# Kernel tuning notes

Measured on AMD Instinct MI355X. Metric: run time of the kernel, lower is better.

Reference implementation:

```python
import jax, jax.numpy as jnp
import numpy as np

N_POINTS = 2048
N_EVENTS = 2_000_000
N_QUAD = 10           # midpoint Riemann samples for the non-event integral
NON_EVENT_WEIGHT = 1.0
EPS = 1e-12           # numerical floor inside sqrt (mirrors torch PairwiseDistance eps)


def setup_inputs() -> dict:
    key = jax.random.key(0)
    k1, k2, k3, k4 = jax.random.split(key, 4)
    # learned parameters, init uniform(-0.25, 0.25) as in init_vector
    z0 = jax.random.uniform(k1, (N_POINTS, 2), minval=-0.25, maxval=0.25)
    v0 = jax.random.uniform(k2, (N_POINTS, 2), minval=-0.25, maxval=0.25)
    beta = jnp.asarray(0.0, jnp.float32)  # background intensity parameter
    # event data: columns [u, v, t] split into int pairs and float times
    data_uv = jax.random.randint(k3, (N_EVENTS, 2), 0, N_POINTS).astype(jnp.int32)
    data_t = jax.random.uniform(k4, (N_EVENTS,), dtype=jnp.float32)
    # all node pairs, lower triangle offset=-1 (matches torch.tril_indices)
    iu, ju = np.tril_indices(N_POINTS, k=-1)
    pair_u = jnp.asarray(iu, jnp.int32)
    pair_v = jnp.asarray(ju, jnp.int32)
    t0 = jnp.asarray(0.0, jnp.float32)
    tn = jnp.asarray(1.0, jnp.float32)
    return dict(z0=z0, v0=v0, beta=beta, data_t=data_t, t0=t0, tn=tn,
                data_uv=data_uv, pair_u=pair_u, pair_v=pair_v)


def reference(z0, v0, beta, data_t, t0, tn, data_uv, pair_u, pair_v):
    # --- event term: sum over events of log lambda_uv(t) = beta - ||z_u(t)-z_v(t)|| ---
    u, v = data_uv[:, 0], data_uv[:, 1]
    # z_i(t) = z0_i + v0_i * t  (constant velocity); difference vector per event [E,2]
    dz = (z0[u] - z0[v]) + (v0[u] - v0[v]) * data_t[:, None]
    event_dist = jnp.sqrt(jnp.sum(dz * dz, axis=-1) + EPS)
    event_intensity = jnp.sum(beta - event_dist)

    # --- non-event term: integral over [t0,tn] of lambda_uv(t) for every node pair ---
    # midpoint Riemann rule with N_QUAD samples
    ts = t0 + (jnp.arange(N_QUAD, dtype=jnp.float32) + 0.5) * (tn - t0) / N_QUAD
    dt = (tn - t0) / N_QUAD
    dz0 = z0[pair_u] - z0[pair_v]          # [P,2]
    dv0 = v0[pair_u] - v0[pair_v]          # [P,2]
    dp = dz0[None] + dv0[None] * ts[:, None, None]   # [T,P,2]
    pair_dist = jnp.sqrt(jnp.sum(dp * dp, axis=-1) + EPS)  # [T,P]
    non_event_intensity = dt * jnp.sum(jnp.exp(beta - pair_dist))

    return event_intensity - NON_EVENT_WEIGHT * non_event_intensity
```

## Files before the change

### kernel.cpp

```cpp
#include <hip/hip_runtime.h>

#define BLOCK   256
#define EB      512
#define TILE    64
#define NQUAD   10
#define EPSF    1e-12f

__global__ __launch_bounds__(BLOCK) void cvm_fused_kernel(
    const float* __restrict__ z0, const float* __restrict__ v0,
    const float* __restrict__ beta_p, const float* __restrict__ data_t,
    const float* __restrict__ t0_p, const float* __restrict__ tn_p,
    const int* __restrict__ data_uv,
    float* __restrict__ partials,
    int n_points, int n_events)
{
    __shared__ float4 smem[2048];
    __shared__ float sred[4];

    const int tid = threadIdx.x;
    const int b   = blockIdx.x;
    float acc = 0.0f;

    if (b < EB) {
        const float2* z2 = (const float2*)z0;
        const float2* v2 = (const float2*)v0;
        for (int k = tid; k < n_points; k += BLOCK) {
            float2 z = z2[k];
            float2 v = v2[k];
            smem[k] = make_float4(z.x, z.y, v.x, v.y);
        }
        __syncthreads();

        const int2* uv = (const int2*)data_uv;
        for (int e = b * BLOCK + tid; e < n_events; e += EB * BLOCK) {
            int2  p  = uv[e];
            float t  = data_t[e];
            float4 Pu = smem[p.x];
            float4 Pv = smem[p.y];
            float dx = (Pu.x - Pv.x) + (Pu.z - Pv.z) * t;
            float dy = (Pu.y - Pv.y) + (Pu.w - Pv.w) * t;
            acc += sqrtf(dx * dx + dy * dy + EPSF);
        }
    } else {
        int p  = b - EB;
        int ti = (int)((sqrtf(8.0f * (float)p + 1.0f) - 1.0f) * 0.5f);
        while ((ti + 1) * (ti + 2) / 2 <= p) ti++;
        while (ti * (ti + 1) / 2 > p)        ti--;
        int tj = p - ti * (ti + 1) / 2;
        int I0 = ti * TILE, J0 = tj * TILE;

        float* sI = (float*)smem;
        float* sJ = sI + 4 * TILE;
        if (tid < 2 * TILE) {
            int   side = tid >> 6;
            int   l    = tid & 63;
            int   g    = (side ? J0 : I0) + l;
            float* s   = side ? sJ : sI;
            s[0 * TILE + l] = z0[2 * g];
            s[1 * TILE + l] = z0[2 * g + 1];
            s[2 * TILE + l] = v0[2 * g];
            s[3 * TILE + l] = v0[2 * g + 1];
        }
        __syncthreads();

        float beta = *beta_p, t0 = *t0_p, tn = *tn_p;
        float dt = (tn - t0) * (1.0f / NQUAD);

        int il = tid & 63;
        int w  = tid >> 6;
        int gi = I0 + il;

        float zix = sI[0 * TILE + il], ziy = sI[1 * TILE + il];
        float vix = sI[2 * TILE + il], viy = sI[3 * TILE + il];

        bool diag = (ti == tj);
        for (int k = 0; k < 16; ++k) {
            int jl = w + 4 * k;
            int gj = J0 + jl;
            float dzx = zix - sJ[0 * TILE + jl];
            float dzy = ziy - sJ[1 * TILE + jl];
            float dvx = vix - sJ[2 * TILE + jl];
            float dvy = viy - sJ[3 * TILE + jl];
            if (!diag || gi > gj) {
                float s = 0.0f;
                #pragma unroll
                for (int q = 0; q < NQUAD; ++q) {
                    float tq = t0 + ((float)q + 0.5f) * dt;
                    float dx = dzx + dvx * tq;
                    float dy = dzy + dvy * tq;
                    float d  = sqrtf(dx * dx + dy * dy + EPSF);
                    s += __expf(beta - d);
                }
                acc += s;
            }
        }
    }

    #pragma unroll
    for (int off = 32; off > 0; off >>= 1)
        acc += __shfl_down(acc, off, 64);
    int wave = tid >> 6, lane = tid & 63;
    if (lane == 0) sred[wave] = acc;
    __syncthreads();
    if (tid == 0)
        partials[b] = sred[0] + sred[1] + sred[2] + sred[3];
}

__global__ __launch_bounds__(BLOCK) void cvm_finalize_kernel(
    const float* __restrict__ partials, int total_blocks,
    const float* __restrict__ beta_p, const float* __restrict__ t0_p,
    const float* __restrict__ tn_p,
    float* __restrict__ out, int n_events)
{
    __shared__ float s_e[4], s_p[4];
    float se = 0.0f, sp = 0.0f;
    for (int i = threadIdx.x; i < total_blocks; i += BLOCK) {
        float v = partials[i];
        if (i < EB) se += v; else sp += v;
    }
    #pragma unroll
    for (int off = 32; off > 0; off >>= 1) {
        se += __shfl_down(se, off, 64);
        sp += __shfl_down(sp, off, 64);
    }
    int wave = threadIdx.x >> 6, lane = threadIdx.x & 63;
    if (lane == 0) { s_e[wave] = se; s_p[wave] = sp; }
    __syncthreads();
    if (threadIdx.x == 0) {
        se = s_e[0] + s_e[1] + s_e[2] + s_e[3];
        sp = s_p[0] + s_p[1] + s_p[2] + s_p[3];
        float beta = *beta_p, t0 = *t0_p, tn = *tn_p;
        float dt = (tn - t0) * (1.0f / NQUAD);
        out[0] = ((float)n_events * beta - se) - dt * sp;
    }
}

extern "C" void kernel_launch(void* const* d_in, const int* in_sizes, int n_in,
                              void* d_out, int out_size, void* d_ws, size_t ws_size,
                              hipStream_t stream)
{
    const float* z0      = (const float*)d_in[0];
    const float* v0      = (const float*)d_in[1];
    const float* beta_p  = (const float*)d_in[2];
    const float* data_t  = (const float*)d_in[3];
    const float* t0_p    = (const float*)d_in[4];
    const float* tn_p    = (const float*)d_in[5];
    const int*   data_uv = (const int*)d_in[6];

    int n_points = in_sizes[0] / 2;
    int n_events = in_sizes[3];
    int nt       = n_points / TILE;
    int pt       = nt * (nt + 1) / 2;
    int total    = EB + pt;

    float* partials = (float*)d_ws;
    float* out      = (float*)d_out;

    cvm_fused_kernel<<<total, BLOCK, 0, stream>>>(
        z0, v0, beta_p, data_t, t0_p, tn_p, data_uv,
        partials, n_points, n_events);
    cvm_finalize_kernel<<<1, BLOCK, 0, stream>>>(
        partials, total, beta_p, t0_p, tn_p, out, n_events);
}
```

Measured before the change: 116.1 us.

## Give every block a slice of both event and pair work, atomic final reduce

Replaces the split of 512 event blocks plus 528 pair-tile blocks with 1040 uniform blocks. Each block loads the full point table, handles a strided slice of events, and, if its index is below the pair-tile count, one pair tile. The finalize kernel is removed in favour of a memset and per-block atomicAdd, and exp(beta) is factored out of the quadrature loop. It also switches to the raw hardware sqrt builtin. The aim is better load balance and one fewer launch, at the cost of every block loading the 32KB table and nondeterministic float atomic summation.

```diff
diff --git a/kernel.cpp b/kernel.cpp
--- a/kernel.cpp
+++ b/kernel.cpp
@@ -1,86 +1,73 @@
 #include <hip/hip_runtime.h>
 
 #define BLOCK   256
-#define EB      512
 #define TILE    64
 #define NQUAD   10
 #define EPSF    1e-12f
+#define NTOTAL  1040
 
-__global__ __launch_bounds__(BLOCK) void cvm_fused_kernel(
+__global__ __launch_bounds__(BLOCK) void cvm_kernel(
     const float* __restrict__ z0, const float* __restrict__ v0,
     const float* __restrict__ beta_p, const float* __restrict__ data_t,
     const float* __restrict__ t0_p, const float* __restrict__ tn_p,
     const int* __restrict__ data_uv,
-    float* __restrict__ partials,
-    int n_points, int n_events)
+    float* __restrict__ out,
+    int n_points, int n_events, int pair_tiles)
 {
-    __shared__ float4 smem[2048];
-    __shared__ float sred[4];
+    __shared__ float4 table[2048];
+    __shared__ float sred[8];
 
     const int tid = threadIdx.x;
     const int b   = blockIdx.x;
-    float acc = 0.0f;
 
-    if (b < EB) {
-        const float2* z2 = (const float2*)z0;
-        const float2* v2 = (const float2*)v0;
-        for (int k = tid; k < n_points; k += BLOCK) {
-            float2 z = z2[k];
-            float2 v = v2[k];
-            smem[k] = make_float4(z.x, z.y, v.x, v.y);
-        }
-        __syncthreads();
+    const float2* z2 = (const float2*)z0;
+    const float2* v2 = (const float2*)v0;
+    for (int k = tid; k < n_points; k += BLOCK) {
+        float2 z = z2[k];
+        float2 v = v2[k];
+        table[k] = make_float4(z.x, z.y, v.x, v.y);
+    }
+    __syncthreads();
 
-        const int2* uv = (const int2*)data_uv;
-        for (int e = b * BLOCK + tid; e < n_events; e += EB * BLOCK) {
-            int2  p  = uv[e];
-            float t  = data_t[e];
-            float4 Pu = smem[p.x];
-            float4 Pv = smem[p.y];
-            float dx = (Pu.x - Pv.x) + (Pu.z - Pv.z) * t;
-            float dy = (Pu.y - Pv.y) + (Pu.w - Pv.w) * t;
-            acc += sqrtf(dx * dx + dy * dy + EPSF);
-        }
-    } else {
-        int p  = b - EB;
-        int ti = (int)((sqrtf(8.0f * (float)p + 1.0f) - 1.0f) * 0.5f);
+    const float beta = *beta_p, t0 = *t0_p, tn = *tn_p;
+    const float dt   = (tn - t0) * (1.0f / NQUAD);
+
+    float acc_e = 0.0f;
+    const int2* uv = (const int2*)data_uv;
+    for (int e = b * BLOCK + tid; e < n_events; e += NTOTAL * BLOCK) {
+        int2  p  = uv[e];
+        float t  = data_t[e];
+        float4 Pu = table[p.x];
+        float4 Pv = table[p.y];
+        float dx = (Pu.x - Pv.x) + (Pu.z - Pv.z) * t;
+        float dy = (Pu.y - Pv.y) + (Pu.w - Pv.w) * t;
+        acc_e += __builtin_amdgcn_sqrtf(dx * dx + dy * dy + EPSF);
+    }
+
+    float acc_p = 0.0f;
+    if (b < pair_tiles) {
+        int p  = b;
+        int ti = (int)((__builtin_amdgcn_sqrtf(8.0f * (float)p + 1.0f) - 1.0f) * 0.5f);
         while ((ti + 1) * (ti + 2) / 2 <= p) ti++;
         while (ti * (ti + 1) / 2 > p)        ti--;
         int tj = p - ti * (ti + 1) / 2;
         int I0 = ti * TILE, J0 = tj * TILE;
 
-        float* sI = (float*)smem;
-        float* sJ = sI + 4 * TILE;
-        if (tid < 2 * TILE) {
-            int   side = tid >> 6;
-            int   l    = tid & 63;
-            int   g    = (side ? J0 : I0) + l;
-            float* s   = side ? sJ : sI;
-            s[0 * TILE + l] = z0[2 * g];
-            s[1 * TILE + l] = z0[2 * g + 1];
-            s[2 * TILE + l] = v0[2 * g];
-            s[3 * TILE + l] = v0[2 * g + 1];
-        }
-        __syncthreads();
-
-        float beta = *beta_p, t0 = *t0_p, tn = *tn_p;
-        float dt = (tn - t0) * (1.0f / NQUAD);
-
         int il = tid & 63;
         int w  = tid >> 6;
         int gi = I0 + il;
 
-        float zix = sI[0 * TILE + il], ziy = sI[1 * TILE + il];
-        float vix = sI[2 * TILE + il], viy = sI[3 * TILE + il];
+        float4 Pi = table[I0 + il];
+        bool diag = (ti == tj);
 
-        bool diag = (ti == tj);
         for (int k = 0; k < 16; ++k) {
             int jl = w + 4 * k;
             int gj = J0 + jl;
-            float dzx = zix - sJ[0 * TILE + jl];
-            float dzy = ziy - sJ[1 * TILE + jl];
-            float dvx = vix - sJ[2 * TILE + jl];
-            float dvy = viy - sJ[3 * TILE + jl];
+            float4 Pj = table[J0 + jl];
+            float dzx = Pi.x - Pj.x;
+            float dzy = Pi.y - Pj.y;
+            float dvx = Pi.z - Pj.z;
+            float dvy = Pi.w - Pj.w;
             if (!diag || gi > gj) {
                 float s = 0.0f;
                 #pragma unroll
@@ -88,50 +75,28 @@
                     float tq = t0 + ((float)q + 0.5f) * dt;
                     float dx = dzx + dvx * tq;
                     float dy = dzy + dvy * tq;
-                    float d  = sqrtf(dx * dx + dy * dy + EPSF);
-                    s += __expf(beta - d);
+                    float d  = __builtin_amdgcn_sqrtf(dx * dx + dy * dy + EPSF);
+                    s += __expf(-d);
                 }
-                acc += s;
+                acc_p += s;
             }
         }
     }
 
     #pragma unroll
-    for (int off = 32; off > 0; off >>= 1)
-        acc += __shfl_down(acc, off, 64);
+    for (int off = 32; off > 0; off >>= 1) {
+        acc_e += __shfl_down(acc_e, off, 64);
+        acc_p += __shfl_down(acc_p, off, 64);
+    }
     int wave = tid >> 6, lane = tid & 63;
-    if (lane == 0) sred[wave] = acc;
+    if (lane == 0) { sred[wave] = acc_e; sred[4 + wave] = acc_p; }
     __syncthreads();
-    if (tid == 0)
-        partials[b] = sred[0] + sred[1] + sred[2] + sred[3];
-}
-
-__global__ __launch_bounds__(BLOCK) void cvm_finalize_kernel(
-    const float* __restrict__ partials, int total_blocks,
-    const float* __restrict__ beta_p, const float* __restrict__ t0_p,
-    const float* __restrict__ tn_p,
-    float* __restrict__ out, int n_events)
-{
-    __shared__ float s_e[4], s_p[4];
-    float se = 0.0f, sp = 0.0f;
-    for (int i = threadIdx.x; i < total_blocks; i += BLOCK) {
-        float v = partials[i];
-        if (i < EB) se += v; else sp += v;
-    }
-    #pragma unroll
-    for (int off = 32; off > 0; off >>= 1) {
-        se += __shfl_down(se, off, 64);
-        sp += __shfl_down(sp, off, 64);
-    }
-    int wave = threadIdx.x >> 6, lane = threadIdx.x & 63;
-    if (lane == 0) { s_e[wave] = se; s_p[wave] = sp; }
-    __syncthreads();
-    if (threadIdx.x == 0) {
-        se = s_e[0] + s_e[1] + s_e[2] + s_e[3];
-        sp = s_p[0] + s_p[1] + s_p[2] + s_p[3];
-        float beta = *beta_p, t0 = *t0_p, tn = *tn_p;
-        float dt = (tn - t0) * (1.0f / NQUAD);
-        out[0] = ((float)n_events * beta - se) - dt * sp;
+    if (tid == 0) {
+        float se = sred[0] + sred[1] + sred[2] + sred[3];
+        float sp = sred[4] + sred[5] + sred[6] + sred[7];
+        float contrib = -se - dt * __expf(beta) * sp;
+        if (b == 0) contrib += (float)n_events * beta;
+        atomicAdd(out, contrib);
     }
 }
 
@@ -151,14 +116,12 @@
     int n_events = in_sizes[3];
     int nt       = n_points / TILE;
     int pt       = nt * (nt + 1) / 2;
-    int total    = EB + pt;
 
-    float* partials = (float*)d_ws;
-    float* out      = (float*)d_out;
+    float* out = (float*)d_out;
 
-    cvm_fused_kernel<<<total, BLOCK, 0, stream>>>(
+    hipMemsetAsync(out, 0, sizeof(float), stream);
+
+    cvm_kernel<<<NTOTAL, BLOCK, 0, stream>>>(
         z0, v0, beta_p, data_t, t0_p, tn_p, data_uv,
-        partials, n_points, n_events);
-    cvm_finalize_kernel<<<1, BLOCK, 0, stream>>>(
-        partials, total, beta_p, t0_p, tn_p, out, n_events);
+        out, n_points, n_events, pt);
 }
```

New measurement: 113.9 us. Within noise of the previous version (-1.9%).
